# Performance work log

Hardware: AMD Instinct MI355X
Metric: run time of the kernel (lower is better)

Reference implementation:

```python
import jax, jax.numpy as jnp
import numpy as np

DILATIONS = (1, 6, 12, 24, 36)
EPS = 1e-5


def conv2d(x, w, dil, pad):
    # x: (N,C,H,W), w: (O,I,3,3) or (O,I,1,1)
    return jax.lax.conv_general_dilated(
        x, w, window_strides=(1, 1), padding=[(pad, pad), (pad, pad)],
        rhs_dilation=(dil, dil), dimension_numbers=('NCHW', 'OIHW', 'NCHW'))


def _bilinear_sample(img, ys, xs):
    # img: (C,H,W); ys, xs: (H,W,9) float sampling coords; zero padding outside.
    C, H, W = img.shape
    y0 = jnp.floor(ys)
    x0 = jnp.floor(xs)
    wy1 = ys - y0
    wx1 = xs - x0
    wy0 = 1.0 - wy1
    wx0 = 1.0 - wx1

    def gather(yi, xi, w):
        valid = (yi >= 0) & (yi < H) & (xi >= 0) & (xi < W)
        yc = jnp.clip(yi, 0, H - 1).astype(jnp.int32)
        xc = jnp.clip(xi, 0, W - 1).astype(jnp.int32)
        v = img[:, yc, xc]  # (C,H,W,9)
        return v * (w * valid)[None]

    return (gather(y0, x0, wy0 * wx0) + gather(y0, x0 + 1, wy0 * wx1)
            + gather(y0 + 1, x0, wy1 * wx0) + gather(y0 + 1, x0 + 1, wy1 * wx1))


def deform_unfold(x, offset, dil, pad):
    # x: (N,C,H,W), offset: (N,18,H,W) interleaved (dy,dx) per 3x3 tap.
    N, C, H, W = x.shape
    ky = jnp.repeat(jnp.arange(3), 3)  # (9,)
    kx = jnp.tile(jnp.arange(3), 3)
    base_y = (jnp.arange(H)[:, None, None] + (ky * dil - pad)).astype(x.dtype)  # (H,1,9)
    base_x = (jnp.arange(W)[None, :, None] + (kx * dil - pad)).astype(x.dtype)  # (1,W,9)
    dy = jnp.transpose(offset[:, 0::2], (0, 2, 3, 1))  # (N,H,W,9)
    dx = jnp.transpose(offset[:, 1::2], (0, 2, 3, 1))
    ys = base_y[None] + dy  # (N,H,W,9)
    xs = base_x[None] + dx
    return jax.vmap(_bilinear_sample)(x, ys, xs)  # (N,C,H,W,9)


def dynamic_head(x, cat_ws, scale_w, gamma, beta):
    N, C, H, W = x.shape
    outs = [x]
    for w, dil in zip(cat_ws, DILATIONS):
        fo = conv2d(x, w, dil, dil)           # (N,27,H,W); pad == dil keeps size
        filt = jax.nn.softmax(jnp.transpose(fo[:, :9], (0, 2, 3, 1)), axis=-1)  # (N,H,W,9)
        off = fo[:, -18:]                      # (N,18,H,W)
        samp = deform_unfold(x, off, dil, dil)  # (N,C,H,W,9)
        outs.append(jnp.einsum('nchwk,nhwk->nchw', samp, filt))
    cat = jnp.concatenate(outs, axis=1)        # (N,6C,H,W)
    y = conv2d(cat, scale_w, 1, 0)             # (N,C,H,W)
    mean = jnp.mean(y, axis=(0, 2, 3))
    var = jnp.var(y, axis=(0, 2, 3))
    y = (y - mean[None, :, None, None]) * jax.lax.rsqrt(var + EPS)[None, :, None, None]
    return y * gamma[None, :, None, None] + beta[None, :, None, None]


def setup_inputs() -> dict:
    key = jax.random.key(0)
    ks = jax.random.split(key, 8)
    C = 512
    x = jax.random.normal(ks[0], (2, C, 64, 64), dtype=jnp.float32)
    cat_ws = [0.02 * jax.random.normal(ks[1 + i], (27, C, 3, 3), dtype=jnp.float32) for i in range(5)]
    scale_w = 0.02 * jax.random.normal(ks[6], (C, 6 * C, 1, 1), dtype=jnp.float32)
    gamma = jnp.ones((C,), dtype=jnp.float32)
    beta = jnp.zeros((C,), dtype=jnp.float32)
    return {'x': x, 'w1': cat_ws[0], 'w2': cat_ws[1], 'w3': cat_ws[2],
            'w4': cat_ws[3], 'w5': cat_ws[4], 'scale_w': scale_w,
            'gamma': gamma, 'beta': beta}


def reference(x, w1, w2, w3, w4, w5, scale_w, gamma, beta):
    return dynamic_head(x, (w1, w2, w3, w4, w5), scale_w, gamma, beta)
```

## Files before the change

### kernel.cpp

```cpp
#include <hip/hip_runtime.h>

typedef short short8 __attribute__((ext_vector_type(8)));
typedef float f32x4 __attribute__((ext_vector_type(4)));

#define CST 3072

__device__ __forceinline__ float bf2f(short s) {
  unsigned u = ((unsigned)(unsigned short)s) << 16;
  return __builtin_bit_cast(float, u);
}
__device__ __forceinline__ short f2bf(float f) {
  unsigned u = __builtin_bit_cast(unsigned, f);
  u = (u + 0x7FFFu + ((u >> 16) & 1u)) >> 16;
  return (short)u;
}
__device__ __forceinline__ void gl16(const short* g, short* l) {
  __builtin_amdgcn_global_load_lds(
      (const __attribute__((address_space(1))) unsigned*)g,
      (__attribute__((address_space(3))) unsigned*)l, 16, 0, 0);
}

__global__ __launch_bounds__(256) void k_init(const float* __restrict__ x,
                                              const float* __restrict__ sw,
                                              const float* __restrict__ w1, const float* __restrict__ w2,
                                              const float* __restrict__ w3, const float* __restrict__ w4,
                                              const float* __restrict__ w5,
                                              short* __restrict__ cat,
                                              short* __restrict__ wbf, short* __restrict__ wdr,
                                              float* __restrict__ stats) {
  __shared__ float tile[64][65];
  int b = blockIdx.x;
  int t = threadIdx.x;
  if (b < 1024) {
    int cblk = b & 7, h = (b >> 3) & 63, n = b >> 9;
    int c0 = cblk * 64;
    int lw = t & 63, grp = t >> 6;
    const float* xp = x + (((size_t)n * 512 + c0) * 64 + h) * 64;
#pragma unroll
    for (int i = 0; i < 16; ++i) {
      int cl = grp * 16 + i;
      tile[cl][lw] = xp[(size_t)cl * 4096 + lw];
    }
    __syncthreads();
    int c8 = t & 7, wq = t >> 3;
    size_t mbase = ((size_t)n * 64 + h) * 64;
#pragma unroll
    for (int it = 0; it < 2; ++it) {
      int w = wq + it * 32;
      short8 o;
#pragma unroll
      for (int j = 0; j < 8; ++j) o[j] = f2bf(tile[c8 * 8 + j][w]);
      *(short8*)(cat + (mbase + w) * CST + c0 + c8 * 8) = o;
    }
  } else if (b < 1792) {
    int i8 = (b - 1024) * 256 + t;
    const float4* sp = (const float4*)(sw + (size_t)i8 * 8);
    float4 f0 = sp[0], f1 = sp[1];
    short8 o;
    o[0] = f2bf(f0.x); o[1] = f2bf(f0.y); o[2] = f2bf(f0.z); o[3] = f2bf(f0.w);
    o[4] = f2bf(f1.x); o[5] = f2bf(f1.y); o[6] = f2bf(f1.z); o[7] = f2bf(f1.w);
    *(short8*)(wbf + (size_t)i8 * 8) = o;
  } else if (b < 4672) {
    int j = (b - 1792) * 256 + t;
    int c = j & 511;
    int t2 = j >> 9;
    int oc = t2 & 31;
    int t3 = t2 >> 5;
    int tap = t3 % 9;
    int di = t3 / 9;
    float v = 0.f;
    if (oc < 27) {
      const float* wp = (di == 0) ? w1 : (di == 1) ? w2 : (di == 2) ? w3 : (di == 3) ? w4 : w5;
      v = wp[((oc * 512 + c) * 3 + tap / 3) * 3 + tap % 3];
    }
    wdr[j] = f2bf(v);
  } else {
    int idx = (b - 4672) * 256 + t;
    stats[idx] = 0.f;
  }
}

__global__ __launch_bounds__(128) void k_conv(const short* __restrict__ xsrc,
                                              const short* __restrict__ wdr_all,
                                              int* __restrict__ ctab) {
  __shared__ short As[64 * 256];
  __shared__ short Bs[32 * 256];
  float (*fo)[32][33] = (float (*)[32][33])(void*)As;
  int tid = threadIdx.x;
  int wave = tid >> 6, lane = tid & 63;
  int l15 = lane & 15, quad = lane >> 4;
  int b = blockIdx.x;
  int di = b >> 7;
  int loc = b & 127;
  const int DIL[5] = {1, 6, 12, 24, 36};
  int d = DIL[di];
  int rid = (loc & 7) * 16 + (loc >> 3);
  int h = rid & 63, n = rid >> 6;
  f32x4 acc[2][2];
  f32x4 zz = {0.f, 0.f, 0.f, 0.f};
#pragma unroll
  for (int i = 0; i < 2; ++i)
#pragma unroll
    for (int j = 0; j < 2; ++j) acc[i][j] = zz;
  const short8 z8 = {0, 0, 0, 0, 0, 0, 0, 0};
  int aoff[16];
  int boff[8];
#pragma unroll
  for (int i = 0; i < 16; ++i) {
    int q = i * 128 + tid;
    int w = q >> 5, ch = q & 31;
    aoff[i] = w * CST + (ch ^ (w & 7)) * 8;
  }
#pragma unroll
  for (int i = 0; i < 8; ++i) {
    int q = i * 128 + tid;
    int oc = q >> 5, ch = q & 31;
    boff[i] = oc * 512 + (ch ^ (oc & 7)) * 8;
  }
  const short* wbase = wdr_all + (size_t)di * 9 * 32 * 512;
  int rowb = (n << 12);
#pragma unroll 1
  for (int kh = 0; kh < 2; ++kh) {
    int lastty = -1;
#pragma unroll
    for (int tap = 0; tap < 9; ++tap) {
      int ty = tap / 3, tx = tap % 3;
      int hh = h + (ty - 1) * d;
      if ((unsigned)hh >= 64u) continue;
      __syncthreads();
      if (ty != lastty) {
        const short* abase = xsrc + (size_t)(rowb + (hh << 6)) * CST + kh * 256;
#pragma unroll
        for (int i = 0; i < 16; ++i)
          gl16(abase + aoff[i], As + (i * 128 + wave * 64) * 8);
        lastty = ty;
      }
      {
        const short* bbase = wbase + tap * 32 * 512 + kh * 256;
#pragma unroll
        for (int i = 0; i < 8; ++i)
          gl16(bbase + boff[i], Bs + (i * 128 + wave * 64) * 8);
      }
      __syncthreads();
      int s0 = wave * 32 + (tx - 1) * d;
#pragma unroll
      for (int ks = 0; ks < 8; ++ks) {
        int c = ks * 4 + quad;
        short8 a[2], bb[2];
#pragma unroll
        for (int mt = 0; mt < 2; ++mt) {
          int wp = s0 + mt * 16 + l15;
          bool ok = (unsigned)wp < 64u;
          int wc = ok ? wp : 0;
          short8 av = *(const short8*)(As + wc * 256 + (c ^ (wc & 7)) * 8);
          a[mt] = ok ? av : z8;
        }
#pragma unroll
        for (int ot = 0; ot < 2; ++ot) {
          int oc = ot * 16 + l15;
          bb[ot] = *(const short8*)(Bs + oc * 256 + (c ^ (oc & 7)) * 8);
        }
#pragma unroll
        for (int mt = 0; mt < 2; ++mt)
#pragma unroll
          for (int ot = 0; ot < 2; ++ot)
            acc[mt][ot] = __builtin_amdgcn_mfma_f32_16x16x32_bf16(a[mt], bb[ot], acc[mt][ot], 0, 0, 0);
      }
    }
  }
  __syncthreads();
#pragma unroll
  for (int mt = 0; mt < 2; ++mt)
#pragma unroll
    for (int ot = 0; ot < 2; ++ot)
#pragma unroll
      for (int r = 0; r < 4; ++r)
        fo[wave][mt * 16 + quad * 4 + r][ot * 16 + l15] = acc[mt][ot][r];
  __syncthreads();
  if (tid < 64) {
    int p = tid;
    float* fp = fo[p >> 5][p & 31];
    float mx = fp[0];
#pragma unroll
    for (int k = 1; k < 9; ++k) mx = fmaxf(mx, fp[k]);
    float s = 0.f, e[9];
#pragma unroll
    for (int k = 0; k < 9; ++k) { e[k] = __expf(fp[k] - mx); s += e[k]; }
    float inv = 1.f / s;
#pragma unroll
    for (int k = 0; k < 9; ++k) fp[k] = e[k] * inv;
  }
  __syncthreads();
#pragma unroll
  for (int rr = 0; rr < 5; ++rr) {
    int task = rr * 128 + tid;
    if (task < 576) {
      int p = task / 9;
      int k = task - p * 9;
      const float* fp = fo[p >> 5][p & 31];
      float f = fp[k];
      float dy = fp[9 + 2 * k];
      float dx = fp[10 + 2 * k];
      float ys = (float)(h + (k / 3 - 1) * d) + dy;
      float xs = (float)(p + (k % 3 - 1) * d) + dx;
      float y0f = floorf(ys), x0f = floorf(xs);
      float wy1 = ys - y0f, wx1 = xs - x0f;
      float wy0 = 1.f - wy1, wx0 = 1.f - wx1;
      int y0 = (int)y0f, x0 = (int)x0f;
      int4 ent;
      int* ep = (int*)&ent;
#pragma unroll
      for (int cy = 0; cy < 2; ++cy)
#pragma unroll
        for (int cx = 0; cx < 2; ++cx) {
          int yy = y0 + cy, xx = x0 + cx;
          bool v = ((unsigned)yy < 64u) && ((unsigned)xx < 64u);
          float wt = f * (cy ? wy1 : wy0) * (cx ? wx1 : wx0);
          int row = v ? (yy * 64 + xx) : 0;
          unsigned wb = v ? (unsigned)(unsigned short)f2bf(wt) : 0u;
          ep[cy * 2 + cx] = row | (int)(wb << 16);
        }
      int mm = rowb + (h << 6) + p;
      ((int4*)ctab)[((size_t)di * 8192 + mm) * 9 + k] = ent;
    }
  }
}

__global__ __launch_bounds__(256, 4) void k_samp(const short* __restrict__ xsrc,
                                                 short* __restrict__ cat,
                                                 const int* __restrict__ ctab) {
  int tid = threadIdx.x;
  int wv = __builtin_amdgcn_readfirstlane(tid >> 6);
  int lane = tid & 63;
  int b = blockIdx.x;
  int di = b >> 11;
  int loc = b & 2047;
  int m = (loc & 7) * 1024 + (loc >> 3) * 4 + wv;
  int n = m >> 12;
  const int4* tp = (const int4*)ctab + ((size_t)di * 8192 + m) * 9;
  const short* xb = xsrc + (size_t)(n << 12) * CST + lane * 8;
  float acc[8] = {0.f, 0.f, 0.f, 0.f, 0.f, 0.f, 0.f, 0.f};
#pragma unroll
  for (int k = 0; k < 9; ++k) {
    int4 e = tp[k];
    const int* ep = (const int*)&e;
#pragma unroll
    for (int c = 0; c < 4; ++c) {
      int dw = ep[c];
      float wt = __builtin_bit_cast(float, (unsigned)dw & 0xFFFF0000u);
      int row = dw & 0xFFFF;
      const short8 vv = *(const short8*)(xb + (size_t)row * CST);
#pragma unroll
      for (int j = 0; j < 8; ++j) acc[j] += wt * bf2f(vv[j]);
    }
  }
  short8 o8;
#pragma unroll
  for (int j = 0; j < 8; ++j) o8[j] = f2bf(acc[j]);
  *(short8*)(cat + (size_t)m * CST + 512 * (di + 1) + lane * 8) = o8;
}

__global__ __launch_bounds__(512, 2) void k_gemm(const short* __restrict__ A,
                                                 const short* __restrict__ B,
                                                 short* __restrict__ Y,
                                                 float* __restrict__ stats) {
  __shared__ short As[2][128 * 64];
  __shared__ short Bs[2][128 * 64];
  __shared__ float sred[128][2];
  int tid = threadIdx.x;
  int wave = tid >> 6, lane = tid & 63;
  int l15 = lane & 15, quad = lane >> 4;
  int bid = blockIdx.x;
  int xcd = bid & 7, g = bid >> 3;
  int mt = xcd * 8 + (g & 7);
  int nt = g >> 3;
  int m0 = mt * 128, n0 = nt * 128;
  int wm = (wave >> 2) * 64;
  int wn = (wave & 3) * 32;
  f32x4 acc[4][2];
  f32x4 zz = {0.f, 0.f, 0.f, 0.f};
#pragma unroll
  for (int i = 0; i < 4; ++i)
#pragma unroll
    for (int j = 0; j < 2; ++j) acc[i][j] = zz;
  int r6 = tid >> 3, c8 = tid & 7;
  int cs = (c8 ^ (r6 & 7)) * 8;
  const short* asrc = A + (size_t)(m0 + r6) * CST + cs;
  const short* bsrc = B + (size_t)(n0 + r6) * CST + cs;
  short* adst = &As[0][0] + tid * 8;
  short* bdst = &Bs[0][0] + tid * 8;
#define STAGE_A(p, u, kc) gl16(asrc + (size_t)(u) * 64 * CST + (kc), adst + (p) * 8192 + (u) * 4096)
#define STAGE_B(p, u, kc) gl16(bsrc + (size_t)(u) * 64 * CST + (kc), bdst + (p) * 8192 + (u) * 4096)
  STAGE_A(0, 0, 0); STAGE_A(0, 1, 0); STAGE_B(0, 0, 0); STAGE_B(0, 1, 0);
  STAGE_A(1, 0, 64); STAGE_A(1, 1, 64); STAGE_B(1, 0, 64); STAGE_B(1, 1, 64);
#pragma unroll 1
  for (int t = 0; t < 48; ++t) {
    int cur = t & 1;
    if (t == 47) { asm volatile("s_waitcnt vmcnt(0)" ::: "memory"); }
    else         { asm volatile("s_waitcnt vmcnt(4)" ::: "memory"); }
    __builtin_amdgcn_s_barrier();
    __builtin_amdgcn_sched_barrier(0);
    const short* Ab = &As[cur][0];
    const short* Bb = &Bs[cur][0];
    short8 a[4][2], bf[2][2];
#pragma unroll
    for (int i = 0; i < 4; ++i) {
      int row = wm + i * 16 + l15;
      const short* rp = Ab + row * 64;
#pragma unroll
      for (int kk = 0; kk < 2; ++kk)
        a[i][kk] = *(const short8*)(rp + ((quad + kk * 4) ^ (row & 7)) * 8);
    }
#pragma unroll
    for (int j = 0; j < 2; ++j) {
      int row = wn + j * 16 + l15;
      const short* rp = Bb + row * 64;
#pragma unroll
      for (int kk = 0; kk < 2; ++kk)
        bf[j][kk] = *(const short8*)(rp + ((quad + kk * 4) ^ (row & 7)) * 8);
    }
    asm volatile("s_waitcnt lgkmcnt(0)" ::: "memory");
    __builtin_amdgcn_sched_barrier(0);
    __builtin_amdgcn_s_barrier();
    __builtin_amdgcn_sched_barrier(0);
    if (t < 46) {
      int kc = (t + 2) * 64;
      STAGE_A(cur, 0, kc); STAGE_A(cur, 1, kc);
      STAGE_B(cur, 0, kc); STAGE_B(cur, 1, kc);
    }
    __builtin_amdgcn_s_setprio(1);
#pragma unroll
    for (int kk = 0; kk < 2; ++kk)
#pragma unroll
      for (int i = 0; i < 4; ++i)
#pragma unroll
        for (int j = 0; j < 2; ++j)
          acc[i][j] = __builtin_amdgcn_mfma_f32_16x16x32_bf16(a[i][kk], bf[j][kk], acc[i][j], 0, 0, 0);
    __builtin_amdgcn_s_setprio(0);
  }
#undef STAGE_A
#undef STAGE_B
  if (tid < 256) ((float*)sred)[tid] = 0.f;
  __syncthreads();
#pragma unroll
  for (int i = 0; i < 4; ++i) {
    int row = m0 + wm + i * 16 + quad * 4;
#pragma unroll
    for (int j = 0; j < 2; ++j) {
      int col = n0 + wn + j * 16 + l15;
#pragma unroll
      for (int r = 0; r < 4; ++r)
        Y[(size_t)(row + r) * 512 + col] = f2bf(acc[i][j][r]);
    }
  }
#pragma unroll
  for (int j = 0; j < 2; ++j) {
    float s = 0.f, q = 0.f;
#pragma unroll
    for (int i = 0; i < 4; ++i)
#pragma unroll
      for (int r = 0; r < 4; ++r) {
        float v = acc[i][j][r];
        s += v; q += v * v;
      }
    int lc = wn + j * 16 + l15;
    atomicAdd(&sred[lc][0], s);
    atomicAdd(&sred[lc][1], q);
  }
  __syncthreads();
  if (tid < 128) {
    atomicAdd(&stats[n0 + tid], sred[tid][0]);
    atomicAdd(&stats[512 + n0 + tid], sred[tid][1]);
  }
}

__global__ __launch_bounds__(256) void k_norm(const short* __restrict__ Y,
                                              const float* __restrict__ stats,
                                              const float* __restrict__ gamma,
                                              const float* __restrict__ beta,
                                              float* __restrict__ out) {
  __shared__ float tile[64][65];
  int b = blockIdx.x;
  int cblk = b & 7, h = (b >> 3) & 63, n = b >> 9;
  int c0 = cblk * 64;
  int t = threadIdx.x;
  size_t mbase = ((size_t)n * 64 + h) * 64;
  int c8 = t & 7, wq = t >> 3;
#pragma unroll
  for (int it = 0; it < 2; ++it) {
    int w = wq + it * 32;
    size_t ro = (mbase + w) * 512 + c0 + c8 * 8;
    short8 a = *(const short8*)(Y + ro);
#pragma unroll
    for (int j = 0; j < 8; ++j) tile[w][c8 * 8 + j] = bf2f(a[j]);
  }
  __syncthreads();
  int w4 = (t & 15) * 4, cg = t >> 4;
  float* op = out + (((size_t)n * 512 + c0) * 64 + h) * 64;
#pragma unroll
  for (int i = 0; i < 4; ++i) {
    int c2 = cg * 4 + i;
    int cc = c0 + c2;
    float mean = stats[cc] * (1.f / 8192.f);
    float var = stats[512 + cc] * (1.f / 8192.f) - mean * mean;
    float Ai = gamma[cc] * rsqrtf(var + 1e-5f);
    float Bi = beta[cc] - mean * Ai;
    float4 o;
    o.x = tile[w4 + 0][c2] * Ai + Bi;
    o.y = tile[w4 + 1][c2] * Ai + Bi;
    o.z = tile[w4 + 2][c2] * Ai + Bi;
    o.w = tile[w4 + 3][c2] * Ai + Bi;
    *(float4*)(op + (size_t)c2 * 4096 + w4) = o;
  }
}

extern "C" void kernel_launch(void* const* d_in, const int* in_sizes, int n_in,
                              void* d_out, int out_size, void* d_ws, size_t ws_size,
                              hipStream_t stream) {
  const float* x  = (const float*)d_in[0];
  const float* w1 = (const float*)d_in[1];
  const float* w2 = (const float*)d_in[2];
  const float* w3 = (const float*)d_in[3];
  const float* w4 = (const float*)d_in[4];
  const float* w5 = (const float*)d_in[5];
  const float* sw = (const float*)d_in[6];
  const float* gamma = (const float*)d_in[7];
  const float* beta  = (const float*)d_in[8];
  float* out = (float*)d_out;

  char* ws = (char*)d_ws;
  short* cat   = (short*)ws;
  short* wbf   = (short*)(ws + 50331648);
  short* wdr   = (short*)(ws + 53477376);
  short* yb    = (short*)(ws + 54951936);
  float* stats = (float*)(ws + 71729152);
  int*   ctab  = (int*)(ws + 71733248);

  k_init<<<4676, 256, 0, stream>>>(x, sw, w1, w2, w3, w4, w5, cat, wbf, wdr, stats);
  k_conv<<<640, 128, 0, stream>>>(cat, wdr, ctab);
  k_samp<<<10240, 256, 0, stream>>>(cat, cat, ctab);
  k_gemm<<<256, 512, 0, stream>>>(cat, wbf, yb, stats);
  k_norm<<<1024, 256, 0, stream>>>(yb, stats, gamma, beta, out);
}
```

Before: 206.3 us.

## Fuse batchnorm into GEMM via grid-wide atomic barrier

Removes the separate normalisation kernel and runs it as an epilogue of the GEMM. After all 256 GEMM blocks have added their column statistics, they meet at a global atomic counter barrier, then each block normalises and transposes four 64x64 tiles into the output. This saves one kernel launch and its tail, and may let Y reads hit in L2. It relies on all 256 blocks being co-resident, since the spin barrier deadlocks otherwise. The counter is placed inside the yb region, which is only safe if Y never reaches that offset.

```diff
diff --git a/kernel.cpp b/kernel.cpp
--- a/kernel.cpp
+++ b/kernel.cpp
@@ -27,7 +27,7 @@
                                               const float* __restrict__ w5,
                                               short* __restrict__ cat,
                                               short* __restrict__ wbf, short* __restrict__ wdr,
-                                              float* __restrict__ stats) {
+                                              float* __restrict__ stats, int* __restrict__ cnt) {
   __shared__ float tile[64][65];
   int b = blockIdx.x;
   int t = threadIdx.x;
@@ -77,6 +77,7 @@
   } else {
     int idx = (b - 4672) * 256 + t;
     stats[idx] = 0.f;
+    if (idx == 0) *cnt = 0;
   }
 }
 
@@ -263,10 +264,15 @@
 __global__ __launch_bounds__(512, 2) void k_gemm(const short* __restrict__ A,
                                                  const short* __restrict__ B,
                                                  short* __restrict__ Y,
-                                                 float* __restrict__ stats) {
-  __shared__ short As[2][128 * 64];
-  __shared__ short Bs[2][128 * 64];
-  __shared__ float sred[128][2];
+                                                 float* __restrict__ stats,
+                                                 const float* __restrict__ gamma,
+                                                 const float* __restrict__ beta,
+                                                 float* __restrict__ out,
+                                                 int* __restrict__ cnt) {
+  __shared__ __align__(16) char smem[66560];
+  short* As = (short*)smem;
+  short* Bs = (short*)(smem + 32768);
+  float (*sred)[2] = (float (*)[2])(smem + 65536);
   int tid = threadIdx.x;
   int wave = tid >> 6, lane = tid & 63;
   int l15 = lane & 15, quad = lane >> 4;
@@ -287,8 +293,8 @@
   int cs = (c8 ^ (r6 & 7)) * 8;
   const short* asrc = A + (size_t)(m0 + r6) * CST + cs;
   const short* bsrc = B + (size_t)(n0 + r6) * CST + cs;
-  short* adst = &As[0][0] + tid * 8;
-  short* bdst = &Bs[0][0] + tid * 8;
+  short* adst = As + tid * 8;
+  short* bdst = Bs + tid * 8;
 #define STAGE_A(p, u, kc) gl16(asrc + (size_t)(u) * 64 * CST + (kc), adst + (p) * 8192 + (u) * 4096)
 #define STAGE_B(p, u, kc) gl16(bsrc + (size_t)(u) * 64 * CST + (kc), bdst + (p) * 8192 + (u) * 4096)
   STAGE_A(0, 0, 0); STAGE_A(0, 1, 0); STAGE_B(0, 0, 0); STAGE_B(0, 1, 0);
@@ -300,8 +306,8 @@
     else         { asm volatile("s_waitcnt vmcnt(4)" ::: "memory"); }
     __builtin_amdgcn_s_barrier();
     __builtin_amdgcn_sched_barrier(0);
-    const short* Ab = &As[cur][0];
-    const short* Bb = &Bs[cur][0];
+    const short* Ab = As + cur * 8192;
+    const short* Bb = Bs + cur * 8192;
     short8 a[4][2], bf[2][2];
 #pragma unroll
     for (int i = 0; i < 4; ++i) {
@@ -372,45 +378,51 @@
     atomicAdd(&stats[n0 + tid], sred[tid][0]);
     atomicAdd(&stats[512 + n0 + tid], sred[tid][1]);
   }
-}
-
-__global__ __launch_bounds__(256) void k_norm(const short* __restrict__ Y,
-                                              const float* __restrict__ stats,
-                                              const float* __restrict__ gamma,
-                                              const float* __restrict__ beta,
-                                              float* __restrict__ out) {
-  __shared__ float tile[64][65];
-  int b = blockIdx.x;
-  int cblk = b & 7, h = (b >> 3) & 63, n = b >> 9;
-  int c0 = cblk * 64;
-  int t = threadIdx.x;
-  size_t mbase = ((size_t)n * 64 + h) * 64;
-  int c8 = t & 7, wq = t >> 3;
-#pragma unroll
-  for (int it = 0; it < 2; ++it) {
-    int w = wq + it * 32;
-    size_t ro = (mbase + w) * 512 + c0 + c8 * 8;
-    short8 a = *(const short8*)(Y + ro);
-#pragma unroll
-    for (int j = 0; j < 8; ++j) tile[w][c8 * 8 + j] = bf2f(a[j]);
-  }
-  __syncthreads();
-  int w4 = (t & 15) * 4, cg = t >> 4;
-  float* op = out + (((size_t)n * 512 + c0) * 64 + h) * 64;
-#pragma unroll
-  for (int i = 0; i < 4; ++i) {
-    int c2 = cg * 4 + i;
-    int cc = c0 + c2;
-    float mean = stats[cc] * (1.f / 8192.f);
-    float var = stats[512 + cc] * (1.f / 8192.f) - mean * mean;
-    float Ai = gamma[cc] * rsqrtf(var + 1e-5f);
-    float Bi = beta[cc] - mean * Ai;
-    float4 o;
-    o.x = tile[w4 + 0][c2] * Ai + Bi;
-    o.y = tile[w4 + 1][c2] * Ai + Bi;
-    o.z = tile[w4 + 2][c2] * Ai + Bi;
-    o.w = tile[w4 + 3][c2] * Ai + Bi;
-    *(float4*)(op + (size_t)c2 * 4096 + w4) = o;
+  __threadfence();
+  __syncthreads();
+  if (tid == 0) {
+    __hip_atomic_fetch_add(cnt, 1, __ATOMIC_ACQ_REL, __HIP_MEMORY_SCOPE_AGENT);
+    while (__hip_atomic_load(cnt, __ATOMIC_ACQUIRE, __HIP_MEMORY_SCOPE_AGENT) < 256)
+      __builtin_amdgcn_s_sleep(8);
+  }
+  __syncthreads();
+  int sub = tid >> 8, tn = tid & 255;
+  float (*ntile)[65] = (float (*)[65])(smem + sub * 16640);
+  int c8n = tn & 7, wqn = tn >> 3;
+  int w4 = (tn & 15) * 4, cg = tn >> 4;
+#pragma unroll 1
+  for (int r = 0; r < 2; ++r) {
+    int tl = g * 4 + r * 2 + sub;
+    int slabg = xcd * 16 + (tl >> 3);
+    int cblk = tl & 7;
+    int nn = slabg >> 6, h = slabg & 63, c0 = cblk * 64;
+    size_t mbase = ((size_t)nn * 64 + h) * 64;
+    __syncthreads();
+#pragma unroll
+    for (int it = 0; it < 2; ++it) {
+      int w = wqn + it * 32;
+      size_t ro = (mbase + w) * 512 + c0 + c8n * 8;
+      short8 av = *(const short8*)(Y + ro);
+#pragma unroll
+      for (int j = 0; j < 8; ++j) ntile[w][c8n * 8 + j] = bf2f(av[j]);
+    }
+    __syncthreads();
+    float* op = out + (((size_t)nn * 512 + c0) * 64 + h) * 64;
+#pragma unroll
+    for (int i = 0; i < 4; ++i) {
+      int c2 = cg * 4 + i;
+      int cc = c0 + c2;
+      float mean = stats[cc] * (1.f / 8192.f);
+      float var = stats[512 + cc] * (1.f / 8192.f) - mean * mean;
+      float Ai = gamma[cc] * rsqrtf(var + 1e-5f);
+      float Bi = beta[cc] - mean * Ai;
+      float4 o;
+      o.x = ntile[w4 + 0][c2] * Ai + Bi;
+      o.y = ntile[w4 + 1][c2] * Ai + Bi;
+      o.z = ntile[w4 + 2][c2] * Ai + Bi;
+      o.w = ntile[w4 + 3][c2] * Ai + Bi;
+      *(float4*)(op + (size_t)c2 * 4096 + w4) = o;
+    }
   }
 }
 
@@ -433,12 +445,12 @@
   short* wbf   = (short*)(ws + 50331648);
   short* wdr   = (short*)(ws + 53477376);
   short* yb    = (short*)(ws + 54951936);
+  int*   cnt   = (int*)(ws + 63340544);
   float* stats = (float*)(ws + 71729152);
   int*   ctab  = (int*)(ws + 71733248);
 
-  k_init<<<4676, 256, 0, stream>>>(x, sw, w1, w2, w3, w4, w5, cat, wbf, wdr, stats);
+  k_init<<<4676, 256, 0, stream>>>(x, sw, w1, w2, w3, w4, w5, cat, wbf, wdr, stats, cnt);
   k_conv<<<640, 128, 0, stream>>>(cat, wdr, ctab);
   k_samp<<<10240, 256, 0, stream>>>(cat, cat, ctab);
-  k_gemm<<<256, 512, 0, stream>>>(cat, wbf, yb, stats);
-  k_norm<<<1024, 256, 0, stream>>>(yb, stats, gamma, beta, out);
-}
+  k_gemm<<<256, 512, 0, stream>>>(cat, wbf, yb, stats, gamma, beta, out, cnt);
+}
```

After: 239.3 us. +16.0%, slower.

## Software-pipeline offset-conv tile loads through registers to overlap with MFMA

Applied to the files above, without the earlier changes.

Replaces direct global-to-LDS loads with register prefetch: the next step's A row tile and B weight tile are loaded into registers while the current step's MFMAs run, then written to LDS at the next iteration start. The tap loop is flattened into a single step loop over the valid rows and both K halves. This is meant to hide global memory latency behind compute. In exchange it adds 24 short8 registers per thread, which may reduce occupancy, and it uses manual barriers and waitcnt.

```diff
diff --git a/kernel.cpp b/kernel.cpp
--- a/kernel.cpp
+++ b/kernel.cpp
@@ -119,53 +119,85 @@
   }
   const short* wbase = wdr_all + (size_t)di * 9 * 32 * 512;
   int rowb = (n << 12);
+  int tyl[3], nty = 0;
+#pragma unroll
+  for (int ty = 0; ty < 3; ++ty) {
+    int hh = h + (ty - 1) * d;
+    if ((unsigned)hh < 64u) tyl[nty++] = ty;
+  }
+  int n3 = 3 * nty;
+  int nstep = 2 * n3;
+  short8 areg[16], breg[8];
+  {
+    int hh = h + (tyl[0] - 1) * d;
+    const short* abase = xsrc + (size_t)(rowb + (hh << 6)) * CST;
+#pragma unroll
+    for (int i = 0; i < 16; ++i) areg[i] = *(const short8*)(abase + aoff[i]);
+    const short* bbase = wbase + (tyl[0] * 3) * 32 * 512;
+#pragma unroll
+    for (int i = 0; i < 8; ++i) breg[i] = *(const short8*)(bbase + boff[i]);
+  }
 #pragma unroll 1
-  for (int kh = 0; kh < 2; ++kh) {
-    int lastty = -1;
-#pragma unroll
-    for (int tap = 0; tap < 9; ++tap) {
-      int ty = tap / 3, tx = tap % 3;
-      int hh = h + (ty - 1) * d;
-      if ((unsigned)hh >= 64u) continue;
-      __syncthreads();
-      if (ty != lastty) {
-        const short* abase = xsrc + (size_t)(rowb + (hh << 6)) * CST + kh * 256;
-#pragma unroll
-        for (int i = 0; i < 16; ++i)
-          gl16(abase + aoff[i], As + (i * 128 + wave * 64) * 8);
-        lastty = ty;
+  for (int s = 0; s < nstep; ++s) {
+    int kh = (s >= n3) ? 1 : 0;
+    int rem = s - kh * n3;
+    int g = rem / 3;
+    int tx = rem - g * 3;
+    __builtin_amdgcn_s_barrier();
+    asm volatile("s_waitcnt vmcnt(0)" ::: "memory");
+    __builtin_amdgcn_sched_barrier(0);
+    if (tx == 0) {
+#pragma unroll
+      for (int i = 0; i < 16; ++i)
+        *(short8*)(As + ((size_t)(i * 128 + tid)) * 8) = areg[i];
+    }
+#pragma unroll
+    for (int i = 0; i < 8; ++i)
+      *(short8*)(Bs + ((size_t)(i * 128 + tid)) * 8) = breg[i];
+    asm volatile("s_waitcnt lgkmcnt(0)" ::: "memory");
+    __builtin_amdgcn_sched_barrier(0);
+    __builtin_amdgcn_s_barrier();
+    if (s + 1 < nstep) {
+      int s2 = s + 1;
+      int kh2 = (s2 >= n3) ? 1 : 0;
+      int rem2 = s2 - kh2 * n3;
+      int g2 = rem2 / 3;
+      int tx2 = rem2 - g2 * 3;
+      int ty2 = tyl[g2];
+      if (tx2 == 0) {
+        int hh2 = h + (ty2 - 1) * d;
+        const short* abase = xsrc + (size_t)(rowb + (hh2 << 6)) * CST + kh2 * 256;
+#pragma unroll
+        for (int i = 0; i < 16; ++i) areg[i] = *(const short8*)(abase + aoff[i]);
       }
-      {
-        const short* bbase = wbase + tap * 32 * 512 + kh * 256;
-#pragma unroll
-        for (int i = 0; i < 8; ++i)
-          gl16(bbase + boff[i], Bs + (i * 128 + wave * 64) * 8);
+      const short* bbase = wbase + (ty2 * 3 + tx2) * 32 * 512 + kh2 * 256;
+#pragma unroll
+      for (int i = 0; i < 8; ++i) breg[i] = *(const short8*)(bbase + boff[i]);
+      __builtin_amdgcn_sched_barrier(0);
+    }
+    int s0 = wave * 32 + (tx - 1) * d;
+#pragma unroll
+    for (int ks = 0; ks < 8; ++ks) {
+      int c = ks * 4 + quad;
+      short8 a[2], bb[2];
+#pragma unroll
+      for (int mt = 0; mt < 2; ++mt) {
+        int wp = s0 + mt * 16 + l15;
+        bool ok = (unsigned)wp < 64u;
+        int wc = ok ? wp : 0;
+        short8 av = *(const short8*)(As + wc * 256 + (c ^ (wc & 7)) * 8);
+        a[mt] = ok ? av : z8;
       }
-      __syncthreads();
-      int s0 = wave * 32 + (tx - 1) * d;
-#pragma unroll
-      for (int ks = 0; ks < 8; ++ks) {
-        int c = ks * 4 + quad;
-        short8 a[2], bb[2];
-#pragma unroll
-        for (int mt = 0; mt < 2; ++mt) {
-          int wp = s0 + mt * 16 + l15;
-          bool ok = (unsigned)wp < 64u;
-          int wc = ok ? wp : 0;
-          short8 av = *(const short8*)(As + wc * 256 + (c ^ (wc & 7)) * 8);
-          a[mt] = ok ? av : z8;
-        }
-#pragma unroll
-        for (int ot = 0; ot < 2; ++ot) {
-          int oc = ot * 16 + l15;
-          bb[ot] = *(const short8*)(Bs + oc * 256 + (c ^ (oc & 7)) * 8);
-        }
-#pragma unroll
-        for (int mt = 0; mt < 2; ++mt)
-#pragma unroll
-          for (int ot = 0; ot < 2; ++ot)
-            acc[mt][ot] = __builtin_amdgcn_mfma_f32_16x16x32_bf16(a[mt], bb[ot], acc[mt][ot], 0, 0, 0);
+#pragma unroll
+      for (int ot = 0; ot < 2; ++ot) {
+        int oc = ot * 16 + l15;
+        bb[ot] = *(const short8*)(Bs + oc * 256 + (c ^ (oc & 7)) * 8);
       }
+#pragma unroll
+      for (int mt = 0; mt < 2; ++mt)
+#pragma unroll
+        for (int ot = 0; ot < 2; ++ot)
+          acc[mt][ot] = __builtin_amdgcn_mfma_f32_16x16x32_bf16(a[mt], bb[ot], acc[mt][ot], 0, 0, 0);
     }
   }
   __syncthreads();
```

Measured after the change: 214.1 us. +3.8%, slower.

## Load GEMM B fragments directly to registers and use 4-wave 64x64 warp tiles

Applied to the files above, without the earlier changes.

The GEMM block shrinks from 8 to 4 waves, each computing a 64x64 sub-tile. The B operand is no longer staged through LDS. Each wave loads its B fragments straight from global memory into registers, double-buffered one step ahead, while A keeps the async global-to-LDS pipeline. This halves LDS traffic and usage, at the cost of more registers per wave and uncoalesced, possibly redundant global B loads across waves. The B load wait is folded into the existing vmcnt accounting, which may not match the new outstanding-load counts.

```diff
diff --git a/kernel.cpp b/kernel.cpp
--- a/kernel.cpp
+++ b/kernel.cpp
@@ -260,12 +260,11 @@
   *(short8*)(cat + (size_t)m * CST + 512 * (di + 1) + lane * 8) = o8;
 }
 
-__global__ __launch_bounds__(512, 2) void k_gemm(const short* __restrict__ A,
+__global__ __launch_bounds__(256, 2) void k_gemm(const short* __restrict__ A,
                                                  const short* __restrict__ B,
                                                  short* __restrict__ Y,
                                                  float* __restrict__ stats) {
-  __shared__ short As[2][128 * 64];
-  __shared__ short Bs[2][128 * 64];
+  __shared__ short As[2 * 128 * 64];
   __shared__ float sred[128][2];
   int tid = threadIdx.x;
   int wave = tid >> 6, lane = tid & 63;
@@ -275,78 +274,88 @@
   int mt = xcd * 8 + (g & 7);
   int nt = g >> 3;
   int m0 = mt * 128, n0 = nt * 128;
-  int wm = (wave >> 2) * 64;
-  int wn = (wave & 3) * 32;
-  f32x4 acc[4][2];
+  int wm = (wave >> 1) * 64;
+  int wn = (wave & 1) * 64;
+  f32x4 acc[4][4];
   f32x4 zz = {0.f, 0.f, 0.f, 0.f};
 #pragma unroll
   for (int i = 0; i < 4; ++i)
 #pragma unroll
-    for (int j = 0; j < 2; ++j) acc[i][j] = zz;
-  int r6 = tid >> 3, c8 = tid & 7;
-  int cs = (c8 ^ (r6 & 7)) * 8;
-  const short* asrc = A + (size_t)(m0 + r6) * CST + cs;
-  const short* bsrc = B + (size_t)(n0 + r6) * CST + cs;
-  short* adst = &As[0][0] + tid * 8;
-  short* bdst = &Bs[0][0] + tid * 8;
-#define STAGE_A(p, u, kc) gl16(asrc + (size_t)(u) * 64 * CST + (kc), adst + (p) * 8192 + (u) * 4096)
-#define STAGE_B(p, u, kc) gl16(bsrc + (size_t)(u) * 64 * CST + (kc), bdst + (p) * 8192 + (u) * 4096)
-  STAGE_A(0, 0, 0); STAGE_A(0, 1, 0); STAGE_B(0, 0, 0); STAGE_B(0, 1, 0);
-  STAGE_A(1, 0, 64); STAGE_A(1, 1, 64); STAGE_B(1, 0, 64); STAGE_B(1, 1, 64);
+    for (int j = 0; j < 4; ++j) acc[i][j] = zz;
+  const short* asrc[4];
+  short* adst[4];
+#pragma unroll
+  for (int it = 0; it < 4; ++it) {
+    int q = it * 256 + tid;
+    int row = q >> 3, c8 = q & 7;
+    asrc[it] = A + (size_t)(m0 + row) * CST + (c8 ^ (row & 7)) * 8;
+    adst[it] = As + q * 8;
+  }
+  const short* bb[4];
+#pragma unroll
+  for (int j = 0; j < 4; ++j)
+    bb[j] = B + (size_t)(n0 + wn + j * 16 + l15) * CST + quad * 8;
+  short8 bA[4][2], bB[4][2];
+#pragma unroll
+  for (int it = 0; it < 4; ++it) gl16(asrc[it], adst[it]);
+#pragma unroll
+  for (int j = 0; j < 4; ++j)
+#pragma unroll
+    for (int kk = 0; kk < 2; ++kk)
+      bA[j][kk] = *(const short8*)(bb[j] + kk * 32);
+#pragma unroll
+  for (int it = 0; it < 4; ++it) gl16(asrc[it] + 64, adst[it] + 8192);
+
+#define GITER(T, BCUR, BNXT)                                                   \
+  {                                                                            \
+    if ((T) == 47) { asm volatile("s_waitcnt vmcnt(0)" ::: "memory"); }        \
+    else           { asm volatile("s_waitcnt vmcnt(4)" ::: "memory"); }        \
+    __builtin_amdgcn_s_barrier();                    \
+    __builtin_amdgcn_sched_barrier(0);                                         \
+    if ((T) + 1 < 48) {                              \
+      _Pragma("unroll") for (int j = 0; j < 4; ++j)                            \
+        _Pragma("unroll") for (int kk = 0; kk < 2; ++kk)                       \
+          BNXT[j][kk] = *(const short8*)(bb[j] + ((T) + 1) * 64 + kk * 32);    \
+    }                                                                          \
+    const short* Ab = As + ((T) & 1) * 8192;                                   \
+    short8 a[4][2];                                                            \
+    _Pragma("unroll") for (int i = 0; i < 4; ++i) {                            \
+      int row = wm + i * 16 + l15;                                             \
+      _Pragma("unroll") for (int kk = 0; kk < 2; ++kk)                         \
+        a[i][kk] = *(const short8*)(Ab + row * 64 +                            \
+                                    ((quad + kk * 4) ^ (row & 7)) * 8);        \
+    }                                                                          \
+    asm volatile("s_waitcnt lgkmcnt(0)" ::: "memory");                         \
+    __builtin_amdgcn_sched_barrier(0);                                         \
+    __builtin_amdgcn_s_barrier();               \
+    __builtin_amdgcn_sched_barrier(0);                                         \
+    if ((T) + 2 < 48) {                          \
+      _Pragma("unroll") for (int it = 0; it < 4; ++it)                         \
+        gl16(asrc[it] + ((T) + 2) * 64, adst[it] + ((T) & 1) * 8192);          \
+    }                                                                          \
+    __builtin_amdgcn_s_setprio(1);                                             \
+    _Pragma("unroll") for (int kk = 0; kk < 2; ++kk)                           \
+      _Pragma("unroll") for (int i = 0; i < 4; ++i)                            \
+        _Pragma("unroll") for (int j = 0; j < 4; ++j)                          \
+          acc[i][j] = __builtin_amdgcn_mfma_f32_16x16x32_bf16(                 \
+              a[i][kk], BCUR[j][kk], acc[i][j], 0, 0, 0);                      \
+    __builtin_amdgcn_s_setprio(0);                                             \
+  }
+
 #pragma unroll 1
-  for (int t = 0; t < 48; ++t) {
-    int cur = t & 1;
-    if (t == 47) { asm volatile("s_waitcnt vmcnt(0)" ::: "memory"); }
-    else         { asm volatile("s_waitcnt vmcnt(4)" ::: "memory"); }
-    __builtin_amdgcn_s_barrier();
-    __builtin_amdgcn_sched_barrier(0);
-    const short* Ab = &As[cur][0];
-    const short* Bb = &Bs[cur][0];
-    short8 a[4][2], bf[2][2];
-#pragma unroll
-    for (int i = 0; i < 4; ++i) {
-      int row = wm + i * 16 + l15;
-      const short* rp = Ab + row * 64;
-#pragma unroll
-      for (int kk = 0; kk < 2; ++kk)
-        a[i][kk] = *(const short8*)(rp + ((quad + kk * 4) ^ (row & 7)) * 8);
-    }
-#pragma unroll
-    for (int j = 0; j < 2; ++j) {
-      int row = wn + j * 16 + l15;
-      const short* rp = Bb + row * 64;
-#pragma unroll
-      for (int kk = 0; kk < 2; ++kk)
-        bf[j][kk] = *(const short8*)(rp + ((quad + kk * 4) ^ (row & 7)) * 8);
-    }
-    asm volatile("s_waitcnt lgkmcnt(0)" ::: "memory");
-    __builtin_amdgcn_sched_barrier(0);
-    __builtin_amdgcn_s_barrier();
-    __builtin_amdgcn_sched_barrier(0);
-    if (t < 46) {
-      int kc = (t + 2) * 64;
-      STAGE_A(cur, 0, kc); STAGE_A(cur, 1, kc);
-      STAGE_B(cur, 0, kc); STAGE_B(cur, 1, kc);
-    }
-    __builtin_amdgcn_s_setprio(1);
-#pragma unroll
-    for (int kk = 0; kk < 2; ++kk)
-#pragma unroll
-      for (int i = 0; i < 4; ++i)
-#pragma unroll
-        for (int j = 0; j < 2; ++j)
-          acc[i][j] = __builtin_amdgcn_mfma_f32_16x16x32_bf16(a[i][kk], bf[j][kk], acc[i][j], 0, 0, 0);
-    __builtin_amdgcn_s_setprio(0);
-  }
-#undef STAGE_A
-#undef STAGE_B
+  for (int tt = 0; tt < 48; tt += 2) {
+    GITER(tt, bA, bB);
+    GITER(tt + 1, bB, bA);
+  }
+#undef GITER
+  __syncthreads();
   if (tid < 256) ((float*)sred)[tid] = 0.f;
   __syncthreads();
 #pragma unroll
   for (int i = 0; i < 4; ++i) {
     int row = m0 + wm + i * 16 + quad * 4;
 #pragma unroll
-    for (int j = 0; j < 2; ++j) {
+    for (int j = 0; j < 4; ++j) {
       int col = n0 + wn + j * 16 + l15;
 #pragma unroll
       for (int r = 0; r < 4; ++r)
@@ -354,7 +363,7 @@
     }
   }
 #pragma unroll
-  for (int j = 0; j < 2; ++j) {
+  for (int j = 0; j < 4; ++j) {
     float s = 0.f, q = 0.f;
 #pragma unroll
     for (int i = 0; i < 4; ++i)
@@ -439,6 +448,6 @@
   k_init<<<4676, 256, 0, stream>>>(x, sw, w1, w2, w3, w4, w5, cat, wbf, wdr, stats);
   k_conv<<<640, 128, 0, stream>>>(cat, wdr, ctab);
   k_samp<<<10240, 256, 0, stream>>>(cat, cat, ctab);
-  k_gemm<<<256, 512, 0, stream>>>(cat, wbf, yb, stats);
+  k_gemm<<<256, 256, 0, stream>>>(cat, wbf, yb, stats);
   k_norm<<<1024, 256, 0, stream>>>(yb, stats, gamma, beta, out);
 }
```

Result: slower. 239.1 us (+15.9%).
